# Kernel optimization log

Measured on AMD Instinct MI355X. Metric: run time of the kernel, lower is better.

## Reference

```python
import jax, jax.numpy as jnp
import numpy as np

# HUSM region -> channel mapping (19 channels, 4 disjoint regions)
REGIONS = [
    [0, 1, 5, 8, 9, 10, 14],    # frontal
    [2, 11, 17],                # central
    [3, 12, 18],                # parietal
    [4, 6, 7, 13, 15, 16],      # occipital
]
N_CHAN = 19
N_REG = 4
_region_id = np.empty(N_CHAN, dtype=np.int32)
for r, chans in enumerate(REGIONS):
    for c in chans:
        _region_id[c] = r
REGION_ID = jnp.array(_region_id)
REGION_COUNTS = jnp.array([len(r) for r in REGIONS], dtype=jnp.float32)

N_HEADS, D_K, D_V, D_MODEL, D_FF = 8, 32, 32, 256, 1024
EPS = 1e-5


def layernorm(x):
    # default nn.LayerNorm: gamma=1, beta=0 (layer re-created each forward)
    mu = jnp.mean(x, axis=-1, keepdims=True)
    var = jnp.var(x, axis=-1, keepdims=True)
    return (x - mu) * jax.lax.rsqrt(var + EPS)


def mha(q_in, k_in, v_in, wq, wk, wv, wo):
    # q_in: [B, S, D]
    B, S, _ = q_in.shape
    Q = jnp.einsum('bsd,dhk->bhsk', q_in, wq.reshape(D_MODEL, N_HEADS, D_K))
    K = jnp.einsum('bsd,dhk->bhsk', k_in, wk.reshape(D_MODEL, N_HEADS, D_K))
    V = jnp.einsum('bsd,dhv->bhsv', v_in, wv.reshape(D_MODEL, N_HEADS, D_V))
    scores = jnp.einsum('bhqk,bhsk->bhqs', Q, K) / jnp.sqrt(jnp.float32(D_K))
    attn = jax.nn.softmax(scores, axis=-1)
    ctx = jnp.einsum('bhqs,bhsv->bqhv', attn, V).reshape(B, S, N_HEADS * D_V)
    return layernorm(ctx @ wo + q_in)


def setup_inputs() -> dict:
    key = jax.random.key(0)
    ks = jax.random.split(key, 12)
    B = 4096
    sc = 1.0 / np.sqrt(D_MODEL)
    inp = {
        'x': jax.random.normal(ks[0], (B, N_CHAN, D_MODEL), dtype=jnp.float32),
        'rsa_wq': jax.random.normal(ks[1], (D_MODEL, D_MODEL), dtype=jnp.float32) * sc,
        'rsa_wk': jax.random.normal(ks[2], (D_MODEL, D_MODEL), dtype=jnp.float32) * sc,
        'rsa_wv': jax.random.normal(ks[3], (D_MODEL, D_MODEL), dtype=jnp.float32) * sc,
        'rsa_wo': jax.random.normal(ks[4], (D_MODEL, D_MODEL), dtype=jnp.float32) * sc,
        'lsa_wq': jax.random.normal(ks[5], (D_MODEL, D_MODEL), dtype=jnp.float32) * sc,
        'lsa_wk': jax.random.normal(ks[6], (D_MODEL, D_MODEL), dtype=jnp.float32) * sc,
        'lsa_wv': jax.random.normal(ks[7], (D_MODEL, D_MODEL), dtype=jnp.float32) * sc,
        'lsa_wo': jax.random.normal(ks[8], (D_MODEL, D_MODEL), dtype=jnp.float32) * sc,
        'ffn_w1': jax.random.normal(ks[9], (D_MODEL, D_FF), dtype=jnp.float32) * sc,
        'ffn_w2': jax.random.normal(ks[10], (D_FF, D_MODEL), dtype=jnp.float32) * (1.0 / np.sqrt(D_FF)),
    }
    return inp


def reference(x, rsa_wq, rsa_wk, rsa_wv, rsa_wo,
              lsa_wq, lsa_wk, lsa_wv, lsa_wo, ffn_w1, ffn_w2):
    # --- region gather + avgpool: mean of channels per region -> [B, 4, D]
    fe_sum = jax.ops.segment_sum(jnp.swapaxes(x, 0, 1), REGION_ID,
                                 num_segments=N_REG)          # [4, B, D]
    fe_region = jnp.swapaxes(fe_sum, 0, 1) / REGION_COUNTS[None, :, None]
    # --- tiny 4-token region self-attention
    refined = mha(fe_region, fe_region, fe_region,
                  rsa_wq, rsa_wk, rsa_wv, rsa_wo)             # [B, 4, D]
    # --- scatter-add refined region feature back to its channels
    x = x + refined[:, REGION_ID, :]                          # [B, 19, D]
    # --- full-channel MHA + FFN
    fused = mha(x, x, x, lsa_wq, lsa_wk, lsa_wv, lsa_wo)
    ffn = jax.nn.relu(fused @ ffn_w1) @ ffn_w2
    return layernorm(ffn + fused)
```

## Files before the change

### kernel.cpp

```cpp
#include <hip/hip_runtime.h>
#include <stdint.h>
#include <stddef.h>


#define DEVINL __device__ __forceinline__

typedef __attribute__((ext_vector_type(8))) short short8;
typedef __attribute__((ext_vector_type(4))) float floatx4;
typedef __attribute__((ext_vector_type(8))) unsigned short ushort8;
typedef __attribute__((ext_vector_type(4))) unsigned short ushort4v;

DEVINL float bf2f(unsigned short u){
  union { unsigned int i; float f; } x; x.i = ((unsigned int)u) << 16; return x.f;
}
DEVINL unsigned short f2bf(float f){
  union { float f; unsigned int i; } x; x.f = f;
  unsigned int r = x.i + 0x7fffu + ((x.i >> 16) & 1u);
  return (unsigned short)(r >> 16);
}

typedef __attribute__((address_space(1))) void gvoid_t;
typedef __attribute__((address_space(3))) void lvoid_t;
DEVINL void gload_lds16(const void* g, void* l){
  __builtin_amdgcn_global_load_lds((gvoid_t*)g, (lvoid_t*)l, 16, 0, 0);
}

__global__ __launch_bounds__(256) void wprep_all(
    const float* __restrict__ rq, const float* __restrict__ rk,
    const float* __restrict__ rv, const float* __restrict__ ro,
    const float* __restrict__ lq, const float* __restrict__ lk,
    const float* __restrict__ lv, const float* __restrict__ lo,
    const float* __restrict__ w1, const float* __restrict__ w2,
    unsigned short* __restrict__ wt)
{
  int idx = blockIdx.x * 256 + threadIdx.x;
  const float* W; unsigned short* D; int N, r;
  const int K = (idx < 786432) ? 256 : 1024;
  if (idx < 524288){
    int wsel = idx >> 16; r = idx & 65535; N = 256; D = wt + wsel * 65536;
    switch (wsel){
      case 0: W = rq; break; case 1: W = rk; break; case 2: W = rv; break; case 3: W = ro; break;
      case 4: W = lq; break; case 5: W = lk; break; case 6: W = lv; break; default: W = lo; break;
    }
  } else if (idx < 786432){
    r = idx - 524288; N = 1024; D = wt + 524288; W = w1;
  } else {
    r = idx - 786432; N = 256; D = wt + 786432; W = w2;
  }
  int k = r / N, n = r - k * N;
  D[(size_t)n * K + k] = f2bf(W[r]);
}

__global__ __launch_bounds__(256) void pool_kernel(const float* __restrict__ x,
                                                   unsigned short* __restrict__ fe)
{
  const int b = blockIdx.x, d = threadIdx.x;
  const float* xb = x + (size_t)b * 4864 + d;
  float s0 = xb[0*256]+xb[1*256]+xb[5*256]+xb[8*256]+xb[9*256]+xb[10*256]+xb[14*256];
  float s1 = xb[2*256]+xb[11*256]+xb[17*256];
  float s2 = xb[3*256]+xb[12*256]+xb[18*256];
  float s3 = xb[4*256]+xb[6*256]+xb[7*256]+xb[13*256]+xb[15*256]+xb[16*256];
  unsigned short* fb = fe + (size_t)b * 1024 + d;
  fb[0]   = f2bf(s0 * (1.f/7.f));
  fb[256] = f2bf(s1 * (1.f/3.f));
  fb[512] = f2bf(s2 * (1.f/3.f));
  fb[768] = f2bf(s3 * (1.f/6.f));
}

template<int RELU>
__global__ __launch_bounds__(256, 3)
void gemm_kernel(const unsigned short* __restrict__ A,
                 const unsigned short* __restrict__ Bt,
                 unsigned short* __restrict__ C, int M, int N, int K)
{
  __shared__ __align__(1024) unsigned short lds[2][8192];
  const int tid  = threadIdx.x;
  const int wave = tid >> 6, lane = tid & 63;
  const int wm = wave >> 1, wn = wave & 1;
  const int rowA0 = blockIdx.x * 128;
  const int rowB0 = blockIdx.y * 128;
  const int stg_row = lane >> 3;
  const int stg_kb  = (((lane & 7) ^ (lane >> 3)) << 4);

  floatx4 acc[4][4];
  #pragma unroll
  for (int i = 0; i < 4; ++i)
    #pragma unroll
    for (int j = 0; j < 4; ++j) acc[i][j] = (floatx4){0.f, 0.f, 0.f, 0.f};

  const int nk = K >> 6;
  for (int kt = 0; kt < nk; ++kt){
    if (kt) __syncthreads();
    const int kbase = kt << 7;
    #pragma unroll
    for (int s = 0; s < 4; ++s){
      int chunk = wave * 4 + s;
      int r = chunk * 8 + stg_row;
      gload_lds16((const char*)(A  + (size_t)(rowA0 + r) * K) + kbase + stg_kb,
                  (char*)(&lds[0][0]) + chunk * 1024);
      gload_lds16((const char*)(Bt + (size_t)(rowB0 + r) * K) + kbase + stg_kb,
                  (char*)(&lds[1][0]) + chunk * 1024);
    }
    __syncthreads();
    const char* As = (const char*)(&lds[0][0]);
    const char* Bs = (const char*)(&lds[1][0]);
    #pragma unroll
    for (int kk = 0; kk < 2; ++kk){
      short8 a[4], b[4];
      #pragma unroll
      for (int i = 0; i < 4; ++i){
        int row = wm * 64 + i * 16 + (lane & 15);
        int kb  = (kk * 64 + ((lane >> 4) << 4)) ^ ((row & 7) << 4);
        a[i] = *(const short8*)(As + row * 128 + kb);
      }
      #pragma unroll
      for (int j = 0; j < 4; ++j){
        int row = wn * 64 + j * 16 + (lane & 15);
        int kb  = (kk * 64 + ((lane >> 4) << 4)) ^ ((row & 7) << 4);
        b[j] = *(const short8*)(Bs + row * 128 + kb);
      }
      #pragma unroll
      for (int i = 0; i < 4; ++i)
        #pragma unroll
        for (int j = 0; j < 4; ++j)
          acc[i][j] = __builtin_amdgcn_mfma_f32_16x16x32_bf16(a[i], b[j], acc[i][j], 0, 0, 0);
    }
  }

  const int cr = (lane >> 4) << 2;
  const int cc = lane & 15;
  #pragma unroll
  for (int i = 0; i < 4; ++i){
    #pragma unroll
    for (int j = 0; j < 4; ++j){
      int r0 = rowA0 + wm * 64 + i * 16 + cr;
      int c0 = rowB0 + wn * 64 + j * 16 + cc;
      #pragma unroll
      for (int r = 0; r < 4; ++r){
        float v = acc[i][j][r];
        if (RELU) v = fmaxf(v, 0.f);
        C[(size_t)(r0 + r) * N + c0] = f2bf(v);
      }
    }
  }
}

template<int OUTF32>
__global__ __launch_bounds__(512, 4)
void gemm_ln_kernel(const unsigned short* __restrict__ A,
                    const unsigned short* __restrict__ Bt,
                    const unsigned short* __restrict__ Res,
                    void* __restrict__ Out, int M, int K)
{
  __shared__ __align__(1024) char lds[2][40960];
  const int tid  = threadIdx.x;
  const int wave = tid >> 6, lane = tid & 63;
  const int wm = wave >> 2, wn = wave & 3;
  const int rowA0 = blockIdx.x * 64;
  const int stg_row = lane >> 3;
  const int stg_kb  = (((lane & 7) ^ (lane >> 3)) << 4);

  floatx4 acc[2][4];
  #pragma unroll
  for (int i = 0; i < 2; ++i)
    #pragma unroll
    for (int j = 0; j < 4; ++j) acc[i][j] = (floatx4){0.f, 0.f, 0.f, 0.f};

  const int nk = K >> 6;
  int cur = 0;
  #pragma unroll
  for (int s = 0; s < 5; ++s){
    int chunk = wave * 5 + s;
    const unsigned short* src = (chunk < 8)
      ? A  + (size_t)(rowA0 + chunk * 8 + stg_row) * K
      : Bt + (size_t)((chunk - 8) * 8 + stg_row) * K;
    gload_lds16((const char*)src + stg_kb, &lds[0][0] + chunk * 1024);
  }
  __syncthreads();

  for (int kt = 0; kt < nk; ++kt){
    if (kt + 1 < nk){
      const int kbase = (kt + 1) << 7;
      #pragma unroll
      for (int s = 0; s < 5; ++s){
        int chunk = wave * 5 + s;
        const unsigned short* src = (chunk < 8)
          ? A  + (size_t)(rowA0 + chunk * 8 + stg_row) * K
          : Bt + (size_t)((chunk - 8) * 8 + stg_row) * K;
        gload_lds16((const char*)src + kbase + stg_kb, &lds[cur ^ 1][0] + chunk * 1024);
      }
    }
    const char* As = &lds[cur][0];
    const char* Bs = &lds[cur][0] + 8192;
    #pragma unroll
    for (int kk = 0; kk < 2; ++kk){
      short8 a[2], b[4];
      #pragma unroll
      for (int i = 0; i < 2; ++i){
        int row = wm * 32 + i * 16 + (lane & 15);
        int kb  = (kk * 64 + ((lane >> 4) << 4)) ^ ((row & 7) << 4);
        a[i] = *(const short8*)(As + row * 128 + kb);
      }
      #pragma unroll
      for (int j = 0; j < 4; ++j){
        int row = wn * 64 + j * 16 + (lane & 15);
        int kb  = (kk * 64 + ((lane >> 4) << 4)) ^ ((row & 7) << 4);
        b[j] = *(const short8*)(Bs + row * 128 + kb);
      }
      #pragma unroll
      for (int i = 0; i < 2; ++i)
        #pragma unroll
        for (int j = 0; j < 4; ++j)
          acc[i][j] = __builtin_amdgcn_mfma_f32_16x16x32_bf16(a[i], b[j], acc[i][j], 0, 0, 0);
    }
    __syncthreads();
    cur ^= 1;
  }

  float* red_s = (float*)&lds[0][0];
  float* red_q = red_s + 256;
  float* mu_a  = red_s + 512;
  float* rs_a  = red_s + 576;
  const int g  = lane >> 4;
  const int cl = lane & 15;
  #pragma unroll
  for (int i = 0; i < 2; ++i){
    #pragma unroll
    for (int r = 0; r < 4; ++r){
      const int rowl = wm * 32 + i * 16 + g * 4 + r;
      float s = 0.f, q = 0.f;
      #pragma unroll
      for (int j = 0; j < 4; ++j){
        float v = acc[i][j][r] +
                  bf2f(Res[(size_t)(rowA0 + rowl) * 256 + wn * 64 + j * 16 + cl]);
        acc[i][j][r] = v;
        s += v; q += v * v;
      }
      #pragma unroll
      for (int off = 1; off < 16; off <<= 1){
        s += __shfl_xor(s, off); q += __shfl_xor(q, off);
      }
      if (cl == 0){ red_s[wn * 64 + rowl] = s; red_q[wn * 64 + rowl] = q; }
    }
  }
  __syncthreads();
  if (tid < 64){
    float S = red_s[tid] + red_s[64 + tid] + red_s[128 + tid] + red_s[192 + tid];
    float Q = red_q[tid] + red_q[64 + tid] + red_q[128 + tid] + red_q[192 + tid];
    float mu = S * (1.f / 256.f);
    float var = Q * (1.f / 256.f) - mu * mu;
    mu_a[tid] = mu;
    rs_a[tid] = rsqrtf(var + 1e-5f);
  }
  __syncthreads();
  #pragma unroll
  for (int i = 0; i < 2; ++i){
    #pragma unroll
    for (int r = 0; r < 4; ++r){
      const int rowl = wm * 32 + i * 16 + g * 4 + r;
      const float mu = mu_a[rowl], rs = rs_a[rowl];
      #pragma unroll
      for (int j = 0; j < 4; ++j){
        float w = (acc[i][j][r] - mu) * rs;
        size_t idx = (size_t)(rowA0 + rowl) * 256 + wn * 64 + j * 16 + cl;
        if (OUTF32) ((float*)Out)[idx] = w;
        else        ((unsigned short*)Out)[idx] = f2bf(w);
      }
    }
  }
}

__global__ __launch_bounds__(256) void attn4_kernel(
    const unsigned short* __restrict__ QKV, unsigned short* __restrict__ ctx)
{
  const int t = threadIdx.x;
  const int lb = t >> 5, u = t & 31, h = u >> 2, q = u & 3;
  const size_t b = (size_t)blockIdx.x * 8 + lb;
  const unsigned short* tb = QKV + b * 4 * 768;

  float qf[32];
  {
    const ushort8* qp = (const ushort8*)(tb + (size_t)q * 768 + h * 32);
    #pragma unroll
    for (int g = 0; g < 4; ++g){
      ushort8 v = qp[g];
      #pragma unroll
      for (int e = 0; e < 8; ++e) qf[g * 8 + e] = bf2f(v[e]);
    }
  }
  float sc[4];
  #pragma unroll
  for (int s = 0; s < 4; ++s){
    const ushort8* kp = (const ushort8*)(tb + (size_t)s * 768 + 256 + h * 32);
    float a0 = 0, a1 = 0, a2 = 0, a3 = 0;
    #pragma unroll
    for (int g = 0; g < 4; ++g){
      ushort8 v = kp[g];
      a0 += qf[g*8+0]*bf2f(v[0]); a1 += qf[g*8+1]*bf2f(v[1]);
      a2 += qf[g*8+2]*bf2f(v[2]); a3 += qf[g*8+3]*bf2f(v[3]);
      a0 += qf[g*8+4]*bf2f(v[4]); a1 += qf[g*8+5]*bf2f(v[5]);
      a2 += qf[g*8+6]*bf2f(v[6]); a3 += qf[g*8+7]*bf2f(v[7]);
    }
    sc[s] = ((a0 + a1) + (a2 + a3)) * 0.17677669529663687f;
  }
  float m = fmaxf(fmaxf(sc[0], sc[1]), fmaxf(sc[2], sc[3]));
  float sum = 0.f;
  #pragma unroll
  for (int s = 0; s < 4; ++s){ sc[s] = __expf(sc[s] - m); sum += sc[s]; }
  float inv = 1.f / sum;

  float o[32];
  #pragma unroll
  for (int d = 0; d < 32; ++d) o[d] = 0.f;
  #pragma unroll
  for (int s = 0; s < 4; ++s){
    float p = sc[s] * inv;
    const ushort8* vp = (const ushort8*)(tb + (size_t)s * 768 + 512 + h * 32);
    #pragma unroll
    for (int g = 0; g < 4; ++g){
      ushort8 v = vp[g];
      #pragma unroll
      for (int e = 0; e < 8; ++e) o[g * 8 + e] += p * bf2f(v[e]);
    }
  }
  unsigned short* cp = ctx + (b * 4 + q) * 256 + h * 32;
  #pragma unroll
  for (int g = 0; g < 4; ++g){
    ushort8 w;
    #pragma unroll
    for (int e = 0; e < 8; ++e) w[e] = f2bf(o[g * 8 + e]);
    ((ushort8*)cp)[g] = w;
  }
}

__global__ __launch_bounds__(256) void scatter_kernel(
    const float* __restrict__ x, const unsigned short* __restrict__ ref,
    unsigned short* __restrict__ x2)
{
  const int b = blockIdx.x, d = threadIdx.x;
  float rv[4];
  #pragma unroll
  for (int r = 0; r < 4; ++r) rv[r] = bf2f(ref[(size_t)b * 1024 + r * 256 + d]);
  const float* xb = x + (size_t)b * 4864 + d;
  unsigned short* xo = x2 + (size_t)b * 4864 + d;
  const int rid[19] = {0,0,1,2,3,0,3,3,0,0,0,1,2,3,0,3,3,1,2};
  #pragma unroll
  for (int c = 0; c < 19; ++c) xo[c * 256] = f2bf(xb[c * 256] + rv[rid[c]]);
}

__global__ __launch_bounds__(304) void attn19_kernel(
    const unsigned short* __restrict__ QKV, unsigned short* __restrict__ ctx)
{
  __shared__ unsigned short KV[38][320];
  const int tid = threadIdx.x;
  const size_t b = blockIdx.x;
  const unsigned short* base = QKV + b * 19 * 768;

  #pragma unroll
  for (int it = 0; it < 4; ++it){
    int c = tid + it * 304;
    int m = (c >= 608);
    int i = c - m * 608;
    int s = i >> 5, j = i & 31;
    ushort8 w = *(const ushort8*)(base + (size_t)s * 768 + 256 + (m << 8) + j * 8);
    int slot = j >> 1;
    unsigned short* dst = &KV[m * 19 + s][slot * 20 + (j & 1) * 8];
    ushort4v lo = {w[0], w[1], w[2], w[3]};
    ushort4v hi = {w[4], w[5], w[6], w[7]};
    *(ushort4v*)dst = lo;
    *(ushort4v*)(dst + 4) = hi;
  }
  __syncthreads();

  const int u = tid;
  const int q = u >> 4, h = (u >> 1) & 7, half = u & 1;
  const int slot = h * 2 + half;
  const int roff = slot * 20;

  float qf[16];
  {
    const ushort8* qp = (const ushort8*)(base + (size_t)q * 768 + h * 32 + half * 16);
    #pragma unroll
    for (int g = 0; g < 2; ++g){
      ushort8 v = qp[g];
      #pragma unroll
      for (int e = 0; e < 8; ++e) qf[g * 8 + e] = bf2f(v[e]);
    }
  }

  float p[19];
  float m = -1e30f;
  #pragma unroll
  for (int s = 0; s < 19; ++s){
    const unsigned short* kr = &KV[s][roff];
    float a0 = 0, a1 = 0, a2 = 0, a3 = 0;
    #pragma unroll
    for (int g = 0; g < 4; ++g){
      ushort4v kvv = *(const ushort4v*)(kr + g * 4);
      a0 += qf[g*4+0] * bf2f(kvv[0]); a1 += qf[g*4+1] * bf2f(kvv[1]);
      a2 += qf[g*4+2] * bf2f(kvv[2]); a3 += qf[g*4+3] * bf2f(kvv[3]);
    }
    float part = (a0 + a1) + (a2 + a3);
    part += __shfl_xor(part, 1);
    p[s] = part * 0.17677669529663687f;
    m = fmaxf(m, p[s]);
  }
  float sum = 0.f;
  #pragma unroll
  for (int s = 0; s < 19; ++s){ p[s] = __expf(p[s] - m); sum += p[s]; }
  float inv = 1.f / sum;

  float o[16];
  #pragma unroll
  for (int d = 0; d < 16; ++d) o[d] = 0.f;
  #pragma unroll
  for (int s = 0; s < 19; ++s){
    float ps = p[s] * inv;
    const unsigned short* vr = &KV[19 + s][roff];
    #pragma unroll
    for (int g = 0; g < 4; ++g){
      ushort4v vv = *(const ushort4v*)(vr + g * 4);
      o[g*4+0] += ps * bf2f(vv[0]); o[g*4+1] += ps * bf2f(vv[1]);
      o[g*4+2] += ps * bf2f(vv[2]); o[g*4+3] += ps * bf2f(vv[3]);
    }
  }
  unsigned short* cp = ctx + (b * 19 + q) * 256 + h * 32 + half * 16;
  #pragma unroll
  for (int g = 0; g < 2; ++g){
    ushort8 w;
    #pragma unroll
    for (int e = 0; e < 8; ++e) w[e] = f2bf(o[g * 8 + e]);
    ((ushort8*)cp)[g] = w;
  }
}

extern "C" void kernel_launch(void* const* d_in, const int* in_sizes, int n_in,
                              void* d_out, int out_size, void* d_ws, size_t ws_size,
                              hipStream_t stream)
{
  (void)n_in; (void)out_size;
  const float* x  = (const float*)d_in[0];
  const float* rq = (const float*)d_in[1];
  const float* rk = (const float*)d_in[2];
  const float* rv = (const float*)d_in[3];
  const float* ro = (const float*)d_in[4];
  const float* lq = (const float*)d_in[5];
  const float* lk = (const float*)d_in[6];
  const float* lv = (const float*)d_in[7];
  const float* lo = (const float*)d_in[8];
  const float* w1 = (const float*)d_in[9];
  const float* w2 = (const float*)d_in[10];

  const int B = in_sizes[0] / 4864;
  const int M4  = B * 4;
  const int M19 = B * 19;
  const int MH  = M19 / 2;
  const size_t MB = 1ull << 20;
  if (ws_size < 240 * MB) return;

  char* ws = (char*)d_ws;
  unsigned short* WT    = (unsigned short*)(ws);
  unsigned short* FE    = (unsigned short*)(ws + 2   * MB);
  unsigned short* QKV4  = (unsigned short*)(ws + 10  * MB);
  unsigned short* CTX4  = (unsigned short*)(ws + 34  * MB);
  unsigned short* REF   = (unsigned short*)(ws + 42  * MB);
  unsigned short* X2    = (unsigned short*)(ws + 50  * MB);
  unsigned short* QKV19 = (unsigned short*)(ws + 88  * MB);
  unsigned short* CTX19 = (unsigned short*)(ws + 202 * MB);
  unsigned short* FUSED = (unsigned short*)(ws + 88  * MB);
  unsigned short* H     = (unsigned short*)(ws + 126 * MB);
  float* out = (float*)d_out;

  wprep_all<<<4096, 256, 0, stream>>>(rq, rk, rv, ro, lq, lk, lv, lo, w1, w2, WT);
  pool_kernel<<<B, 256, 0, stream>>>(x, FE);
  gemm_kernel<0><<<dim3(M4/128, 6), 256, 0, stream>>>(FE, WT, QKV4, M4, 768, 256);
  attn4_kernel<<<B/8, 256, 0, stream>>>(QKV4, CTX4);
  gemm_ln_kernel<0><<<M4/64, 512, 0, stream>>>(CTX4, WT + 3*65536, FE, REF, M4, 256);
  scatter_kernel<<<B, 256, 0, stream>>>(x, REF, X2);
  gemm_kernel<0><<<dim3(M19/128, 6), 256, 0, stream>>>(X2, WT + 4*65536, QKV19, M19, 768, 256);
  attn19_kernel<<<B, 304, 0, stream>>>(QKV19, CTX19);
  gemm_ln_kernel<0><<<M19/64, 512, 0, stream>>>(CTX19, WT + 7*65536, X2, FUSED, M19, 256);
  for (int hf = 0; hf < 2; ++hf){
    const unsigned short* Fh = FUSED + (size_t)hf * MH * 256;
    gemm_kernel<1><<<dim3(MH/128, 8), 256, 0, stream>>>(Fh, WT + 524288, H, MH, 1024, 256);
    gemm_ln_kernel<1><<<MH/64, 512, 0, stream>>>(H, WT + 786432, Fh,
                                                 out + (size_t)hf * MH * 256, MH, 1024);
  }
}
```

Baseline: 416.3 us.

## Use persistent GEMM with LDS-resident weights and split attn19 across more threads

Replaces the tiled GEMM with a persistent kernel. Each block loads its full 128x256 weight slice into LDS once, then loops over M tiles, reading A fragments straight from global memory into registers instead of staging them through LDS. This removes repeated weight staging and the per-k-tile barriers, at the cost of uncoalesced direct A loads and lower occupancy (64KB LDS, launch bound 2). The attn19 kernel also doubles its thread count to 608, with each thread handling 8 dims instead of 16 and an extra shuffle for the reduction, which adds parallelism and cuts per-thread registers.

```diff
diff --git a/kernel.cpp b/kernel.cpp
--- a/kernel.cpp
+++ b/kernel.cpp
@@ -68,55 +68,54 @@
 }
 
 template<int RELU>
-__global__ __launch_bounds__(256, 3)
-void gemm_kernel(const unsigned short* __restrict__ A,
-                 const unsigned short* __restrict__ Bt,
-                 unsigned short* __restrict__ C, int M, int N, int K)
-{
-  __shared__ __align__(1024) unsigned short lds[2][8192];
+__global__ __launch_bounds__(256, 2)
+void gemm_pw_kernel(const unsigned short* __restrict__ A,
+                    const unsigned short* __restrict__ Bt,
+                    unsigned short* __restrict__ C,
+                    int N, int mtiles)
+{
+  __shared__ __align__(1024) unsigned short Wl[4][8192];
   const int tid  = threadIdx.x;
   const int wave = tid >> 6, lane = tid & 63;
   const int wm = wave >> 1, wn = wave & 1;
-  const int rowA0 = blockIdx.x * 128;
   const int rowB0 = blockIdx.y * 128;
   const int stg_row = lane >> 3;
   const int stg_kb  = (((lane & 7) ^ (lane >> 3)) << 4);
-
-  floatx4 acc[4][4];
-  #pragma unroll
-  for (int i = 0; i < 4; ++i)
-    #pragma unroll
-    for (int j = 0; j < 4; ++j) acc[i][j] = (floatx4){0.f, 0.f, 0.f, 0.f};
-
-  const int nk = K >> 6;
-  for (int kt = 0; kt < nk; ++kt){
-    if (kt) __syncthreads();
-    const int kbase = kt << 7;
-    #pragma unroll
-    for (int s = 0; s < 4; ++s){
-      int chunk = wave * 4 + s;
-      int r = chunk * 8 + stg_row;
-      gload_lds16((const char*)(A  + (size_t)(rowA0 + r) * K) + kbase + stg_kb,
-                  (char*)(&lds[0][0]) + chunk * 1024);
-      gload_lds16((const char*)(Bt + (size_t)(rowB0 + r) * K) + kbase + stg_kb,
-                  (char*)(&lds[1][0]) + chunk * 1024);
-    }
-    __syncthreads();
-    const char* As = (const char*)(&lds[0][0]);
-    const char* Bs = (const char*)(&lds[1][0]);
-    #pragma unroll
-    for (int kk = 0; kk < 2; ++kk){
+  const int K = 256;
+
+  #pragma unroll
+  for (int s = 0; s < 16; ++s){
+    int c = wave * 16 + s;
+    int p = c >> 4;
+    int g = c & 15;
+    int r = g * 8 + stg_row;
+    gload_lds16((const char*)(Bt + (size_t)(rowB0 + r) * K) + p * 128 + stg_kb,
+                (char*)(&Wl[p][0]) + g * 1024);
+  }
+  __syncthreads();
+
+  const int aro = wm * 64 + (lane & 15);
+  const int ako = (lane >> 4) << 3;
+
+  for (int mt = blockIdx.x; mt < mtiles; mt += gridDim.x){
+    const int rowA0 = mt * 128;
+    floatx4 acc[4][4];
+    #pragma unroll
+    for (int i = 0; i < 4; ++i)
+      #pragma unroll
+      for (int j = 0; j < 4; ++j) acc[i][j] = (floatx4){0.f, 0.f, 0.f, 0.f};
+
+    #pragma unroll
+    for (int kk = 0; kk < 8; ++kk){
+      const char* Bs = (const char*)(&Wl[kk >> 1][0]);
       short8 a[4], b[4];
       #pragma unroll
-      for (int i = 0; i < 4; ++i){
-        int row = wm * 64 + i * 16 + (lane & 15);
-        int kb  = (kk * 64 + ((lane >> 4) << 4)) ^ ((row & 7) << 4);
-        a[i] = *(const short8*)(As + row * 128 + kb);
-      }
+      for (int i = 0; i < 4; ++i)
+        a[i] = *(const short8*)(A + (size_t)(rowA0 + aro + i * 16) * K + kk * 32 + ako);
       #pragma unroll
       for (int j = 0; j < 4; ++j){
         int row = wn * 64 + j * 16 + (lane & 15);
-        int kb  = (kk * 64 + ((lane >> 4) << 4)) ^ ((row & 7) << 4);
+        int kb  = (((kk & 1) << 6) + ((lane >> 4) << 4)) ^ ((row & 7) << 4);
         b[j] = *(const short8*)(Bs + row * 128 + kb);
       }
       #pragma unroll
@@ -125,21 +124,21 @@
         for (int j = 0; j < 4; ++j)
           acc[i][j] = __builtin_amdgcn_mfma_f32_16x16x32_bf16(a[i], b[j], acc[i][j], 0, 0, 0);
     }
-  }
-
-  const int cr = (lane >> 4) << 2;
-  const int cc = lane & 15;
-  #pragma unroll
-  for (int i = 0; i < 4; ++i){
-    #pragma unroll
-    for (int j = 0; j < 4; ++j){
-      int r0 = rowA0 + wm * 64 + i * 16 + cr;
-      int c0 = rowB0 + wn * 64 + j * 16 + cc;
-      #pragma unroll
-      for (int r = 0; r < 4; ++r){
-        float v = acc[i][j][r];
-        if (RELU) v = fmaxf(v, 0.f);
-        C[(size_t)(r0 + r) * N + c0] = f2bf(v);
+
+    const int cr = (lane >> 4) << 2;
+    const int cc = lane & 15;
+    #pragma unroll
+    for (int i = 0; i < 4; ++i){
+      #pragma unroll
+      for (int j = 0; j < 4; ++j){
+        int r0 = rowA0 + wm * 64 + i * 16 + cr;
+        int c0 = rowB0 + wn * 64 + j * 16 + cc;
+        #pragma unroll
+        for (int r = 0; r < 4; ++r){
+          float v = acc[i][j][r];
+          if (RELU) v = fmaxf(v, 0.f);
+          C[(size_t)(r0 + r) * N + c0] = f2bf(v);
+        }
       }
     }
   }
@@ -348,7 +347,7 @@
   for (int c = 0; c < 19; ++c) xo[c * 256] = f2bf(xb[c * 256] + rv[rid[c]]);
 }
 
-__global__ __launch_bounds__(304) void attn19_kernel(
+__global__ __launch_bounds__(608) void attn19_kernel(
     const unsigned short* __restrict__ QKV, unsigned short* __restrict__ ctx)
 {
   __shared__ unsigned short KV[38][320];
@@ -357,8 +356,8 @@
   const unsigned short* base = QKV + b * 19 * 768;
 
   #pragma unroll
-  for (int it = 0; it < 4; ++it){
-    int c = tid + it * 304;
+  for (int it = 0; it < 2; ++it){
+    int c = tid + it * 608;
     int m = (c >= 608);
     int i = c - m * 608;
     int s = i >> 5, j = i & 31;
@@ -372,20 +371,16 @@
   }
   __syncthreads();
 
-  const int u = tid;
-  const int q = u >> 4, h = (u >> 1) & 7, half = u & 1;
-  const int slot = h * 2 + half;
-  const int roff = slot * 20;
-
-  float qf[16];
+  const int q  = tid >> 5;
+  const int h  = (tid >> 2) & 7;
+  const int qt = tid & 3;
+  const int roff = (h * 2 + (qt >> 1)) * 20 + (qt & 1) * 8;
+
+  float qf[8];
   {
-    const ushort8* qp = (const ushort8*)(base + (size_t)q * 768 + h * 32 + half * 16);
-    #pragma unroll
-    for (int g = 0; g < 2; ++g){
-      ushort8 v = qp[g];
-      #pragma unroll
-      for (int e = 0; e < 8; ++e) qf[g * 8 + e] = bf2f(v[e]);
-    }
+    ushort8 v = *(const ushort8*)(base + (size_t)q * 768 + h * 32 + qt * 8);
+    #pragma unroll
+    for (int e = 0; e < 8; ++e) qf[e] = bf2f(v[e]);
   }
 
   float p[19];
@@ -393,15 +388,15 @@
   #pragma unroll
   for (int s = 0; s < 19; ++s){
     const unsigned short* kr = &KV[s][roff];
-    float a0 = 0, a1 = 0, a2 = 0, a3 = 0;
-    #pragma unroll
-    for (int g = 0; g < 4; ++g){
-      ushort4v kvv = *(const ushort4v*)(kr + g * 4);
-      a0 += qf[g*4+0] * bf2f(kvv[0]); a1 += qf[g*4+1] * bf2f(kvv[1]);
-      a2 += qf[g*4+2] * bf2f(kvv[2]); a3 += qf[g*4+3] * bf2f(kvv[3]);
-    }
+    ushort4v k0 = *(const ushort4v*)(kr);
+    ushort4v k1 = *(const ushort4v*)(kr + 4);
+    float a0 = qf[0]*bf2f(k0[0]) + qf[4]*bf2f(k1[0]);
+    float a1 = qf[1]*bf2f(k0[1]) + qf[5]*bf2f(k1[1]);
+    float a2 = qf[2]*bf2f(k0[2]) + qf[6]*bf2f(k1[2]);
+    float a3 = qf[3]*bf2f(k0[3]) + qf[7]*bf2f(k1[3]);
     float part = (a0 + a1) + (a2 + a3);
     part += __shfl_xor(part, 1);
+    part += __shfl_xor(part, 2);
     p[s] = part * 0.17677669529663687f;
     m = fmaxf(m, p[s]);
   }
@@ -410,28 +405,24 @@
   for (int s = 0; s < 19; ++s){ p[s] = __expf(p[s] - m); sum += p[s]; }
   float inv = 1.f / sum;
 
-  float o[16];
-  #pragma unroll
-  for (int d = 0; d < 16; ++d) o[d] = 0.f;
+  float o[8];
+  #pragma unroll
+  for (int d = 0; d < 8; ++d) o[d] = 0.f;
   #pragma unroll
   for (int s = 0; s < 19; ++s){
     float ps = p[s] * inv;
     const unsigned short* vr = &KV[19 + s][roff];
-    #pragma unroll
-    for (int g = 0; g < 4; ++g){
-      ushort4v vv = *(const ushort4v*)(vr + g * 4);
-      o[g*4+0] += ps * bf2f(vv[0]); o[g*4+1] += ps * bf2f(vv[1]);
-      o[g*4+2] += ps * bf2f(vv[2]); o[g*4+3] += ps * bf2f(vv[3]);
-    }
-  }
-  unsigned short* cp = ctx + (b * 19 + q) * 256 + h * 32 + half * 16;
-  #pragma unroll
-  for (int g = 0; g < 2; ++g){
-    ushort8 w;
-    #pragma unroll
-    for (int e = 0; e < 8; ++e) w[e] = f2bf(o[g * 8 + e]);
-    ((ushort8*)cp)[g] = w;
-  }
+    ushort4v v0 = *(const ushort4v*)(vr);
+    ushort4v v1 = *(const ushort4v*)(vr + 4);
+    o[0] += ps * bf2f(v0[0]); o[1] += ps * bf2f(v0[1]);
+    o[2] += ps * bf2f(v0[2]); o[3] += ps * bf2f(v0[3]);
+    o[4] += ps * bf2f(v1[0]); o[5] += ps * bf2f(v1[1]);
+    o[6] += ps * bf2f(v1[2]); o[7] += ps * bf2f(v1[3]);
+  }
+  ushort8 w;
+  #pragma unroll
+  for (int e = 0; e < 8; ++e) w[e] = f2bf(o[e]);
+  *(ushort8*)(ctx + (b * 19 + q) * 256 + h * 32 + qt * 8) = w;
 }
 
 extern "C" void kernel_launch(void* const* d_in, const int* in_sizes, int n_in,
@@ -471,18 +462,20 @@
   unsigned short* H     = (unsigned short*)(ws + 126 * MB);
   float* out = (float*)d_out;
 
+  auto pw_gx = [](int mtiles, int ny){ int g = 512 / ny; if (g > mtiles) g = mtiles; if (g < 1) g = 1; return g; };
+
   wprep_all<<<4096, 256, 0, stream>>>(rq, rk, rv, ro, lq, lk, lv, lo, w1, w2, WT);
   pool_kernel<<<B, 256, 0, stream>>>(x, FE);
-  gemm_kernel<0><<<dim3(M4/128, 6), 256, 0, stream>>>(FE, WT, QKV4, M4, 768, 256);
+  gemm_pw_kernel<0><<<dim3(pw_gx(M4/128, 6), 6), 256, 0, stream>>>(FE, WT, QKV4, 768, M4/128);
   attn4_kernel<<<B/8, 256, 0, stream>>>(QKV4, CTX4);
   gemm_ln_kernel<0><<<M4/64, 512, 0, stream>>>(CTX4, WT + 3*65536, FE, REF, M4, 256);
   scatter_kernel<<<B, 256, 0, stream>>>(x, REF, X2);
-  gemm_kernel<0><<<dim3(M19/128, 6), 256, 0, stream>>>(X2, WT + 4*65536, QKV19, M19, 768, 256);
-  attn19_kernel<<<B, 304, 0, stream>>>(QKV19, CTX19);
+  gemm_pw_kernel<0><<<dim3(pw_gx(M19/128, 6), 6), 256, 0, stream>>>(X2, WT + 4*65536, QKV19, 768, M19/128);
+  attn19_kernel<<<B, 608, 0, stream>>>(QKV19, CTX19);
   gemm_ln_kernel<0><<<M19/64, 512, 0, stream>>>(CTX19, WT + 7*65536, X2, FUSED, M19, 256);
   for (int hf = 0; hf < 2; ++hf){
     const unsigned short* Fh = FUSED + (size_t)hf * MH * 256;
-    gemm_kernel<1><<<dim3(MH/128, 8), 256, 0, stream>>>(Fh, WT + 524288, H, MH, 1024, 256);
+    gemm_pw_kernel<1><<<dim3(pw_gx(MH/128, 8), 8), 256, 0, stream>>>(Fh, WT + 524288, H, 1024, MH/128);
     gemm_ln_kernel<1><<<MH/64, 512, 0, stream>>>(H, WT + 786432, Fh,
                                                  out + (size_t)hf * MH * 256, MH, 1024);
   }
```

Measured after the change: 475.4 us. +14.2%, slower.

## Split QKV projection output into separate Q/K/V buffers and rework attention

Applied to the files above, without the earlier changes.

The QKV GEMM epilogue now writes Q, K and V into three separate contiguous [M,256] buffers instead of one interleaved [M,768] tensor. Both attention kernels read from these planar buffers. attn19 is rewritten to stage K and V for the batch element into LDS as fp32, with one thread per (head, query) computing the full 32-wide dot products, which drops the half-split shuffle. In exchange, attn19 now uses about 38KB of LDS per block, up from about 24KB, and leaves 104 of its 256 threads idle after staging, which may hurt occupancy.

```diff
diff --git a/kernel.cpp b/kernel.cpp
--- a/kernel.cpp
+++ b/kernel.cpp
@@ -67,11 +67,14 @@
   fb[768] = f2bf(s3 * (1.f/6.f));
 }
 
-template<int RELU>
+template<int RELU, int SPLIT>
 __global__ __launch_bounds__(256, 3)
 void gemm_kernel(const unsigned short* __restrict__ A,
                  const unsigned short* __restrict__ Bt,
-                 unsigned short* __restrict__ C, int M, int N, int K)
+                 unsigned short* __restrict__ C0,
+                 unsigned short* __restrict__ C1,
+                 unsigned short* __restrict__ C2,
+                 int M, int N, int K)
 {
   __shared__ __align__(1024) unsigned short lds[2][8192];
   const int tid  = threadIdx.x;
@@ -127,6 +130,16 @@
     }
   }
 
+  unsigned short* dst;
+  int colb, ldc;
+  if (SPLIT){
+    const int seg = rowB0 >> 8;
+    dst = (seg == 0) ? C0 : (seg == 1) ? C1 : C2;
+    colb = rowB0 & 255;
+    ldc = 256;
+  } else {
+    dst = C0; colb = rowB0; ldc = N;
+  }
   const int cr = (lane >> 4) << 2;
   const int cc = lane & 15;
   #pragma unroll
@@ -134,12 +147,12 @@
     #pragma unroll
     for (int j = 0; j < 4; ++j){
       int r0 = rowA0 + wm * 64 + i * 16 + cr;
-      int c0 = rowB0 + wn * 64 + j * 16 + cc;
+      int c0 = colb + wn * 64 + j * 16 + cc;
       #pragma unroll
       for (int r = 0; r < 4; ++r){
         float v = acc[i][j][r];
         if (RELU) v = fmaxf(v, 0.f);
-        C[(size_t)(r0 + r) * N + c0] = f2bf(v);
+        dst[(size_t)(r0 + r) * ldc + c0] = f2bf(v);
       }
     }
   }
@@ -271,16 +284,17 @@
 }
 
 __global__ __launch_bounds__(256) void attn4_kernel(
-    const unsigned short* __restrict__ QKV, unsigned short* __restrict__ ctx)
+    const unsigned short* __restrict__ Q, const unsigned short* __restrict__ K,
+    const unsigned short* __restrict__ V, unsigned short* __restrict__ ctx)
 {
   const int t = threadIdx.x;
   const int lb = t >> 5, u = t & 31, h = u >> 2, q = u & 3;
   const size_t b = (size_t)blockIdx.x * 8 + lb;
-  const unsigned short* tb = QKV + b * 4 * 768;
+  const size_t base = b * 1024 + h * 32;
 
   float qf[32];
   {
-    const ushort8* qp = (const ushort8*)(tb + (size_t)q * 768 + h * 32);
+    const ushort8* qp = (const ushort8*)(Q + base + q * 256);
     #pragma unroll
     for (int g = 0; g < 4; ++g){
       ushort8 v = qp[g];
@@ -291,7 +305,7 @@
   float sc[4];
   #pragma unroll
   for (int s = 0; s < 4; ++s){
-    const ushort8* kp = (const ushort8*)(tb + (size_t)s * 768 + 256 + h * 32);
+    const ushort8* kp = (const ushort8*)(K + base + s * 256);
     float a0 = 0, a1 = 0, a2 = 0, a3 = 0;
     #pragma unroll
     for (int g = 0; g < 4; ++g){
@@ -315,7 +329,7 @@
   #pragma unroll
   for (int s = 0; s < 4; ++s){
     float p = sc[s] * inv;
-    const ushort8* vp = (const ushort8*)(tb + (size_t)s * 768 + 512 + h * 32);
+    const ushort8* vp = (const ushort8*)(V + base + s * 256);
     #pragma unroll
     for (int g = 0; g < 4; ++g){
       ushort8 v = vp[g];
@@ -323,7 +337,7 @@
       for (int e = 0; e < 8; ++e) o[g * 8 + e] += p * bf2f(v[e]);
     }
   }
-  unsigned short* cp = ctx + (b * 4 + q) * 256 + h * 32;
+  unsigned short* cp = ctx + base + q * 256;
   #pragma unroll
   for (int g = 0; g < 4; ++g){
     ushort8 w;
@@ -348,61 +362,43 @@
   for (int c = 0; c < 19; ++c) xo[c * 256] = f2bf(xb[c * 256] + rv[rid[c]]);
 }
 
-__global__ __launch_bounds__(304) void attn19_kernel(
-    const unsigned short* __restrict__ QKV, unsigned short* __restrict__ ctx)
-{
-  __shared__ unsigned short KV[38][320];
-  const int tid = threadIdx.x;
+__global__ __launch_bounds__(256) void attn19_kernel(
+    const unsigned short* __restrict__ Q, const unsigned short* __restrict__ K,
+    const unsigned short* __restrict__ V, unsigned short* __restrict__ ctx)
+{
+  __shared__ float Kl[4864];
+  __shared__ float Vl[4864];
   const size_t b = blockIdx.x;
-  const unsigned short* base = QKV + b * 19 * 768;
-
-  #pragma unroll
-  for (int it = 0; it < 4; ++it){
-    int c = tid + it * 304;
-    int m = (c >= 608);
-    int i = c - m * 608;
-    int s = i >> 5, j = i & 31;
-    ushort8 w = *(const ushort8*)(base + (size_t)s * 768 + 256 + (m << 8) + j * 8);
-    int slot = j >> 1;
-    unsigned short* dst = &KV[m * 19 + s][slot * 20 + (j & 1) * 8];
-    ushort4v lo = {w[0], w[1], w[2], w[3]};
-    ushort4v hi = {w[4], w[5], w[6], w[7]};
-    *(ushort4v*)dst = lo;
-    *(ushort4v*)(dst + 4) = hi;
-  }
+  const unsigned short* Kb = K + b * 4864;
+  const unsigned short* Vb = V + b * 4864;
+  for (int i = threadIdx.x; i < 4864; i += 256){ Kl[i] = bf2f(Kb[i]); Vl[i] = bf2f(Vb[i]); }
   __syncthreads();
-
-  const int u = tid;
-  const int q = u >> 4, h = (u >> 1) & 7, half = u & 1;
-  const int slot = h * 2 + half;
-  const int roff = slot * 20;
-
-  float qf[16];
+  const int t = threadIdx.x;
+  if (t >= 152) return;
+  const int h = t / 19, qq = t - h * 19;
+
+  float qf[32];
   {
-    const ushort8* qp = (const ushort8*)(base + (size_t)q * 768 + h * 32 + half * 16);
-    #pragma unroll
-    for (int g = 0; g < 2; ++g){
+    const ushort8* qp = (const ushort8*)(Q + b * 4864 + qq * 256 + h * 32);
+    #pragma unroll
+    for (int g = 0; g < 4; ++g){
       ushort8 v = qp[g];
       #pragma unroll
       for (int e = 0; e < 8; ++e) qf[g * 8 + e] = bf2f(v[e]);
     }
   }
-
   float p[19];
   float m = -1e30f;
   #pragma unroll
   for (int s = 0; s < 19; ++s){
-    const unsigned short* kr = &KV[s][roff];
+    const float* kr = &Kl[s * 256 + h * 32];
     float a0 = 0, a1 = 0, a2 = 0, a3 = 0;
     #pragma unroll
-    for (int g = 0; g < 4; ++g){
-      ushort4v kvv = *(const ushort4v*)(kr + g * 4);
-      a0 += qf[g*4+0] * bf2f(kvv[0]); a1 += qf[g*4+1] * bf2f(kvv[1]);
-      a2 += qf[g*4+2] * bf2f(kvv[2]); a3 += qf[g*4+3] * bf2f(kvv[3]);
-    }
-    float part = (a0 + a1) + (a2 + a3);
-    part += __shfl_xor(part, 1);
-    p[s] = part * 0.17677669529663687f;
+    for (int d = 0; d < 32; d += 4){
+      a0 += qf[d+0] * kr[d+0]; a1 += qf[d+1] * kr[d+1];
+      a2 += qf[d+2] * kr[d+2]; a3 += qf[d+3] * kr[d+3];
+    }
+    p[s] = ((a0 + a1) + (a2 + a3)) * 0.17677669529663687f;
     m = fmaxf(m, p[s]);
   }
   float sum = 0.f;
@@ -410,23 +406,19 @@
   for (int s = 0; s < 19; ++s){ p[s] = __expf(p[s] - m); sum += p[s]; }
   float inv = 1.f / sum;
 
-  float o[16];
-  #pragma unroll
-  for (int d = 0; d < 16; ++d) o[d] = 0.f;
+  float o[32];
+  #pragma unroll
+  for (int d = 0; d < 32; ++d) o[d] = 0.f;
   #pragma unroll
   for (int s = 0; s < 19; ++s){
     float ps = p[s] * inv;
-    const unsigned short* vr = &KV[19 + s][roff];
-    #pragma unroll
-    for (int g = 0; g < 4; ++g){
-      ushort4v vv = *(const ushort4v*)(vr + g * 4);
-      o[g*4+0] += ps * bf2f(vv[0]); o[g*4+1] += ps * bf2f(vv[1]);
-      o[g*4+2] += ps * bf2f(vv[2]); o[g*4+3] += ps * bf2f(vv[3]);
-    }
-  }
-  unsigned short* cp = ctx + (b * 19 + q) * 256 + h * 32 + half * 16;
-  #pragma unroll
-  for (int g = 0; g < 2; ++g){
+    const float* vr = &Vl[s * 256 + h * 32];
+    #pragma unroll
+    for (int d = 0; d < 32; ++d) o[d] += ps * vr[d];
+  }
+  unsigned short* cp = ctx + b * 4864 + qq * 256 + h * 32;
+  #pragma unroll
+  for (int g = 0; g < 4; ++g){
     ushort8 w;
     #pragma unroll
     for (int e = 0; e < 8; ++e) w[e] = f2bf(o[g * 8 + e]);
@@ -461,11 +453,15 @@
   char* ws = (char*)d_ws;
   unsigned short* WT    = (unsigned short*)(ws);
   unsigned short* FE    = (unsigned short*)(ws + 2   * MB);
-  unsigned short* QKV4  = (unsigned short*)(ws + 10  * MB);
+  unsigned short* Q4    = (unsigned short*)(ws + 10  * MB);
+  unsigned short* K4    = (unsigned short*)(ws + 18  * MB);
+  unsigned short* V4    = (unsigned short*)(ws + 26  * MB);
   unsigned short* CTX4  = (unsigned short*)(ws + 34  * MB);
   unsigned short* REF   = (unsigned short*)(ws + 42  * MB);
   unsigned short* X2    = (unsigned short*)(ws + 50  * MB);
-  unsigned short* QKV19 = (unsigned short*)(ws + 88  * MB);
+  unsigned short* Q19   = (unsigned short*)(ws + 88  * MB);
+  unsigned short* K19   = (unsigned short*)(ws + 126 * MB);
+  unsigned short* V19   = (unsigned short*)(ws + 164 * MB);
   unsigned short* CTX19 = (unsigned short*)(ws + 202 * MB);
   unsigned short* FUSED = (unsigned short*)(ws + 88  * MB);
   unsigned short* H     = (unsigned short*)(ws + 126 * MB);
@@ -473,16 +469,16 @@
 
   wprep_all<<<4096, 256, 0, stream>>>(rq, rk, rv, ro, lq, lk, lv, lo, w1, w2, WT);
   pool_kernel<<<B, 256, 0, stream>>>(x, FE);
-  gemm_kernel<0><<<dim3(M4/128, 6), 256, 0, stream>>>(FE, WT, QKV4, M4, 768, 256);
-  attn4_kernel<<<B/8, 256, 0, stream>>>(QKV4, CTX4);
+  gemm_kernel<0,1><<<dim3(M4/128, 6), 256, 0, stream>>>(FE, WT, Q4, K4, V4, M4, 768, 256);
+  attn4_kernel<<<B/8, 256, 0, stream>>>(Q4, K4, V4, CTX4);
   gemm_ln_kernel<0><<<M4/64, 512, 0, stream>>>(CTX4, WT + 3*65536, FE, REF, M4, 256);
   scatter_kernel<<<B, 256, 0, stream>>>(x, REF, X2);
-  gemm_kernel<0><<<dim3(M19/128, 6), 256, 0, stream>>>(X2, WT + 4*65536, QKV19, M19, 768, 256);
-  attn19_kernel<<<B, 304, 0, stream>>>(QKV19, CTX19);
+  gemm_kernel<0,1><<<dim3(M19/128, 6), 256, 0, stream>>>(X2, WT + 4*65536, Q19, K19, V19, M19, 768, 256);
+  attn19_kernel<<<B, 256, 0, stream>>>(Q19, K19, V19, CTX19);
   gemm_ln_kernel<0><<<M19/64, 512, 0, stream>>>(CTX19, WT + 7*65536, X2, FUSED, M19, 256);
   for (int hf = 0; hf < 2; ++hf){
     const unsigned short* Fh = FUSED + (size_t)hf * MH * 256;
-    gemm_kernel<1><<<dim3(MH/128, 8), 256, 0, stream>>>(Fh, WT + 524288, H, MH, 1024, 256);
+    gemm_kernel<1,0><<<dim3(MH/128, 8), 256, 0, stream>>>(Fh, WT + 524288, H, nullptr, nullptr, MH, 1024, 256);
     gemm_ln_kernel<1><<<MH/64, 512, 0, stream>>>(H, WT + 786432, Fh,
                                                  out + (size_t)hf * MH * 256, MH, 1024);
   }
```

Result: faster. 387.3 us (-7.0%).
